# Kernel tuning notes

Hardware: AMD Instinct MI355X
Metric: run time of the kernel (lower is better)

## Reference

```python
import jax, jax.numpy as jnp
import numpy as np

L, B, S, D, H, F = 4, 2, 2048, 768, 12, 3072
HD = D // H
EPS = 1e-5


def _ln(x, g, b):
    m = jnp.mean(x, axis=-1, keepdims=True)
    v = jnp.mean((x - m) ** 2, axis=-1, keepdims=True)
    return (x - m) * jax.lax.rsqrt(v + EPS) * g + b


def setup_inputs() -> dict:
    key = jax.random.key(0)
    ks = jax.random.split(key, 12)
    s = 0.02
    n = lambda k, shp: jax.random.normal(k, shp, jnp.float32) * s
    return {
        "inputs": jax.random.normal(ks[0], (B, S, D), jnp.float32),
        "attn_mask": jax.random.randint(ks[1], (B, S, S), 0, 2) == 1,
        "Wq": n(ks[2], (L, D, D)), "bq": jnp.zeros((L, D), jnp.float32),
        "Wk": n(ks[3], (L, D, D)), "bk": jnp.zeros((L, D), jnp.float32),
        "Wv": n(ks[4], (L, D, D)), "bv": jnp.zeros((L, D), jnp.float32),
        "Wo": n(ks[5], (L, D, D)), "bo": jnp.zeros((L, D), jnp.float32),
        "ln1_g": jnp.ones((L, D), jnp.float32), "ln1_b": jnp.zeros((L, D), jnp.float32),
        "W1": n(ks[6], (L, F, D)), "b1": jnp.zeros((L, F), jnp.float32),
        "W2": n(ks[7], (L, D, F)), "b2": jnp.zeros((L, D), jnp.float32),
        "ln2_g": jnp.ones((L, D), jnp.float32), "ln2_b": jnp.zeros((L, D), jnp.float32),
    }


def reference(inputs, attn_mask, Wq, bq, Wk, bk, Wv, bv, Wo, bo,
              ln1_g, ln1_b, W1, b1, W2, b2, ln2_g, ln2_b):
    x = inputs
    scale = 1.0 / (HD ** 0.5)
    mask = attn_mask[:, None, :, :]  # [B,1,S,S] broadcasts over heads
    nlayers = Wq.shape[0]
    for i in range(nlayers):
        # torch Linear: y = x @ W.T + b, W stored [out,in]
        q = (jnp.einsum('bsd,ed->bse', x, Wq[i]) + bq[i]).reshape(B, S, H, HD)
        k = (jnp.einsum('bsd,ed->bse', x, Wk[i]) + bk[i]).reshape(B, S, H, HD)
        v = (jnp.einsum('bsd,ed->bse', x, Wv[i]) + bv[i]).reshape(B, S, H, HD)
        scores = jnp.einsum('bqhd,bkhd->bhqk', q, k) * scale
        scores = jnp.where(mask, jnp.float32(-1e9), scores)
        p = jax.nn.softmax(scores, axis=-1)
        ctx = jnp.einsum('bhqk,bkhd->bqhd', p, v).reshape(B, S, D)
        attn = jnp.einsum('bsd,ed->bse', ctx, Wo[i]) + bo[i]
        x = _ln(attn + x, ln1_g[i], ln1_b[i])
        h = jax.nn.relu(jnp.einsum('bsd,fd->bsf', x, W1[i]) + b1[i])
        ff = jnp.einsum('bsf,df->bsd', h, W2[i]) + b2[i]
        x = _ln(ff + x, ln2_g[i], ln2_b[i])
    return x
```

## Files before the change

### kernel.cpp

```cpp
#include <hip/hip_runtime.h>
#include <cmath>
#include <cstdint>
#include <cstddef>


typedef __bf16 bf16_t;
typedef __bf16 bf16x8 __attribute__((ext_vector_type(8)));
typedef __bf16 bf16x4 __attribute__((ext_vector_type(4)));
typedef float  f32x4  __attribute__((ext_vector_type(4)));
typedef float  f32x16 __attribute__((ext_vector_type(16)));
typedef int    i32x2  __attribute__((ext_vector_type(2)));

#define DEV static __device__ __forceinline__

constexpr int Lc = 4, Bc = 2, Sc = 2048, Dc = 768, Hc = 12, Fc = 3072, HDc = 64;
constexpr int Mrows = Bc * Sc;
#define QSCALE 0.18033688011112042f

DEV f32x4 mfma16(bf16x8 a, bf16x8 b, f32x4 c) {
  return __builtin_amdgcn_mfma_f32_16x16x32_bf16(a, b, c, 0, 0, 0);
}
DEV f32x16 mfma32(bf16x8 a, bf16x8 b, f32x16 c) {
  return __builtin_amdgcn_mfma_f32_32x32x16_bf16(a, b, c, 0, 0, 0);
}

DEV void gload_lds16(const void* g, void* l) {
  __builtin_amdgcn_global_load_lds(
      (const __attribute__((address_space(1))) void*)g,
      (__attribute__((address_space(3))) void*)l,
      16, 0, 0);
}

DEV float fexp2(float x) { return __builtin_amdgcn_exp2f(x); }

DEV unsigned cvtpk(float lo, float hi_) {
  unsigned r;
  asm("v_cvt_pk_bf16_f32 %0, %1, %2" : "=v"(r) : "v"(lo), "v"(hi_));
  return r;
}
DEV void swapl(unsigned &a, unsigned &b) {
  i32x2 r = __builtin_amdgcn_permlane32_swap((int)a, (int)b, false, false);
  a = (unsigned)r[0];
  b = (unsigned)r[1];
}
DEV bf16x8 frag4(unsigned a, unsigned b, unsigned c, unsigned d) {
  union { unsigned u[4]; bf16x8 v; } x;
  x.u[0] = a; x.u[1] = b; x.u[2] = c; x.u[3] = d;
  return x.v;
}


__global__ __launch_bounds__(256) void cvt_weights_kernel(
    const float* __restrict__ Wq, const float* __restrict__ Wk,
    const float* __restrict__ Wv, const float* __restrict__ Wo,
    const float* __restrict__ W1, const float* __restrict__ W2,
    bf16_t* __restrict__ wqkv, bf16_t* __restrict__ wo,
    bf16_t* __restrict__ w1, bf16_t* __restrict__ w2) {
  constexpr int DD = Dc * Dc;
  constexpr int nDD = Lc * DD;
  constexpr int nFD = Lc * Fc * Dc;
  int i = (blockIdx.x * 256 + threadIdx.x) * 4;
  const float* src;
  bf16_t* dst;
  if (i < 3 * nDD) {
    int sub = i / nDD, r = i - sub * nDD;
    int l = r / DD, off = r - l * DD;
    src = (sub == 0 ? Wq : (sub == 1 ? Wk : Wv)) + r;
    dst = wqkv + (size_t)(l * 3 + sub) * DD + off;
  } else if (i < 4 * nDD) {
    int r = i - 3 * nDD;
    src = Wo + r; dst = wo + r;
  } else if (i < 4 * nDD + nFD) {
    int r = i - 4 * nDD;
    src = W1 + r; dst = w1 + r;
  } else {
    int r = i - 4 * nDD - nFD;
    src = W2 + r; dst = w2 + r;
  }
  float4 v = *(const float4*)src;
  bf16x4 o;
  o[0] = (bf16_t)v.x; o[1] = (bf16_t)v.y; o[2] = (bf16_t)v.z; o[3] = (bf16_t)v.w;
  *(bf16x4*)dst = o;
}

__global__ __launch_bounds__(256) void init_x_kernel(const float* __restrict__ in,
                                                     float* __restrict__ x,
                                                     bf16_t* __restrict__ xb, int n) {
  int i = (blockIdx.x * 256 + threadIdx.x) * 4;
  if (i + 3 < n) {
    float4 v = *(const float4*)(in + i);
    *(float4*)(x + i) = v;
    bf16x4 o;
    o[0] = (bf16_t)v.x; o[1] = (bf16_t)v.y; o[2] = (bf16_t)v.z; o[3] = (bf16_t)v.w;
    *(bf16x4*)(xb + i) = o;
  }
}

__global__ __launch_bounds__(256) void mask_packT_kernel(const int* __restrict__ m,
                                                         unsigned long long* __restrict__ bits) {
  size_t gid = (size_t)blockIdx.x * 256 + threadIdx.x;
  int l = (int)(gid & 63);
  size_t widx = gid >> 6;
  size_t q = widx & (Sc - 1);
  size_t bkw = widx >> 11;
  size_t kw = bkw & (Sc / 64 - 1);
  size_t b = bkw >> 5;
  unsigned long long bm = __ballot(m[(b * Sc + q) * Sc + kw * 64 + l] != 0);
  if (l == 0) bits[widx] = bm;
}

__global__ __launch_bounds__(256) void gemm_ffn1(const bf16_t* __restrict__ A,
                                                 const bf16_t* __restrict__ Bm,
                                                 const float* __restrict__ bias,
                                                 bf16_t* __restrict__ Cb,
                                                 int M, int N, int K) {
  constexpr int BM = 128;
  __shared__ bf16_t sA[BM * 64];
  __shared__ bf16_t sB[128 * 64];
  const int tid = threadIdx.x;
  const int w = tid >> 6, l = tid & 63, lg = l >> 4, li = l & 15;
  const int wr = w >> 1, wc = w & 1;
  const int nwg = gridDim.x, cpx = nwg >> 3;
  const int id = blockIdx.x;
  const int tid2 = (id & 7) * cpx + (id >> 3);
  const int nbx = M / BM;
  const int tm = (tid2 % nbx) * BM, tn = (tid2 / nbx) * 128;

  f32x4 acc[4][4];
#pragma unroll
  for (int m = 0; m < 4; m++)
#pragma unroll
    for (int n = 0; n < 4; n++) acc[m][n] = (f32x4){0.f, 0.f, 0.f, 0.f};

  for (int k0 = 0; k0 < K; k0 += 64) {
#pragma unroll
    for (int i = 0; i < 4; i++) {
      int off = i * 2048 + tid * 8;
      gload_lds16(A + (size_t)(tm + (off >> 6)) * K + k0 + (off & 63),
                  &sA[i * 2048 + w * 512]);
    }
#pragma unroll
    for (int i = 0; i < 4; i++) {
      int off = i * 2048 + tid * 8;
      gload_lds16(Bm + (size_t)(tn + (off >> 6)) * K + k0 + (off & 63),
                  &sB[i * 2048 + w * 512]);
    }
    __syncthreads();
#pragma unroll
    for (int kk = 0; kk < 2; kk++) {
      bf16x8 af[4], bfr[4];
#pragma unroll
      for (int m = 0; m < 4; m++)
        af[m] = *(const bf16x8*)&sA[(wr * 64 + m * 16 + li) * 64 + kk * 32 + lg * 8];
#pragma unroll
      for (int n = 0; n < 4; n++)
        bfr[n] = *(const bf16x8*)&sB[(wc * 64 + n * 16 + li) * 64 + kk * 32 + lg * 8];
#pragma unroll
      for (int m = 0; m < 4; m++)
#pragma unroll
        for (int n = 0; n < 4; n++)
          acc[m][n] = mfma16(af[m], bfr[n], acc[m][n]);
    }
    __syncthreads();
  }

#pragma unroll
  for (int m = 0; m < 4; m++) {
    int rbase = tm + wr * 64 + m * 16 + lg * 4;
#pragma unroll
    for (int n = 0; n < 4; n++) {
      int c = tn + wc * 64 + n * 16 + li;
      float bv = bias[c];
#pragma unroll
      for (int j = 0; j < 4; j++)
        Cb[(size_t)(rbase + j) * N + c] = (bf16_t)fmaxf(acc[m][n][j] + bv, 0.f);
    }
  }
}

__global__ __launch_bounds__(256) void gemm_sk(const bf16_t* __restrict__ A,
                                               const bf16_t* __restrict__ Bm,
                                               float* __restrict__ P0,
                                               float* __restrict__ P1,
                                               int M, int N, int K) {
  __shared__ bf16_t sA[2 * 64 * 64];
  __shared__ bf16_t sB[2 * 128 * 64];
  const int tid = threadIdx.x;
  const int w = tid >> 6, l = tid & 63, lg = l >> 4, li = l & 15;
  const int wr = w >> 1, wc = w & 1;
  const int nwg = gridDim.x, cpx = nwg >> 3;
  const int id = blockIdx.x;
  const int tid2 = (id & 7) * cpx + (id >> 3);
  const int half = nwg >> 1;
  const int ks = tid2 >= half ? 1 : 0;
  const int r = tid2 - ks * half;
  const int nbx = M / 64;
  const int tm = (r % nbx) * 64, tn = (r / nbx) * 128;
  const int kB = K >> 1;
  const int k0base = ks * kB;
  const int nk = kB >> 6;
  float* __restrict__ P = ks ? P1 : P0;

  f32x4 acc[2][4];
#pragma unroll
  for (int m = 0; m < 2; m++)
#pragma unroll
    for (int n = 0; n < 4; n++) acc[m][n] = (f32x4){0.f, 0.f, 0.f, 0.f};

  auto stage = [&](int buf, int kt) {
    const int k0 = k0base + kt * 64;
#pragma unroll
    for (int i = 0; i < 2; i++) {
      int off = i * 2048 + tid * 8;
      gload_lds16(A + (size_t)(tm + (off >> 6)) * K + k0 + (off & 63),
                  &sA[buf * 4096 + i * 2048 + w * 512]);
    }
#pragma unroll
    for (int i = 0; i < 4; i++) {
      int off = i * 2048 + tid * 8;
      gload_lds16(Bm + (size_t)(tn + (off >> 6)) * K + k0 + (off & 63),
                  &sB[buf * 8192 + i * 2048 + w * 512]);
    }
  };

  stage(0, 0);
  asm volatile("s_waitcnt vmcnt(0)" ::: "memory");
  __builtin_amdgcn_s_barrier();
  asm volatile("" ::: "memory");
  int cur = 0;
  for (int kt = 0; kt < nk; kt++) {
    if (kt + 1 < nk) stage(cur ^ 1, kt + 1);
    const bf16_t* sAb = &sA[cur * 4096];
    const bf16_t* sBb = &sB[cur * 8192];
#pragma unroll
    for (int kk = 0; kk < 2; kk++) {
      bf16x8 af[2], bfr[4];
#pragma unroll
      for (int m = 0; m < 2; m++)
        af[m] = *(const bf16x8*)&sAb[(wr * 32 + m * 16 + li) * 64 + kk * 32 + lg * 8];
#pragma unroll
      for (int n = 0; n < 4; n++)
        bfr[n] = *(const bf16x8*)&sBb[(wc * 64 + n * 16 + li) * 64 + kk * 32 + lg * 8];
#pragma unroll
      for (int m = 0; m < 2; m++)
#pragma unroll
        for (int n = 0; n < 4; n++)
          acc[m][n] = mfma16(af[m], bfr[n], acc[m][n]);
    }
    asm volatile("s_waitcnt vmcnt(0)" ::: "memory");
    __builtin_amdgcn_s_barrier();
    asm volatile("" ::: "memory");
    cur ^= 1;
  }

#pragma unroll
  for (int m = 0; m < 2; m++) {
    int rbase = tm + wr * 32 + m * 16 + lg * 4;
#pragma unroll
    for (int n = 0; n < 4; n++) {
      int c = tn + wc * 64 + n * 16 + li;
#pragma unroll
      for (int j = 0; j < 4; j++)
        P[(size_t)(rbase + j) * N + c] = acc[m][n][j];
    }
  }
}

__global__ __launch_bounds__(256) void gemm_qkv(const bf16_t* __restrict__ A,
                                                const bf16_t* __restrict__ Bm,
                                                const float* __restrict__ bq,
                                                const float* __restrict__ bk,
                                                const float* __restrict__ bv,
                                                bf16_t* __restrict__ qo,
                                                bf16_t* __restrict__ ko,
                                                bf16_t* __restrict__ vTo) {
  constexpr int K = Dc;
  __shared__ bf16_t sA[128 * 64];
  __shared__ bf16_t sB[128 * 64];
  const int tid = threadIdx.x;
  const int w = tid >> 6, l = tid & 63, lg = l >> 4, li = l & 15;
  const int wr = w >> 1, wc = w & 1;
  const int nwg = gridDim.x, cpx = nwg >> 3;
  const int id = blockIdx.x;
  const int tid2 = (id & 7) * cpx + (id >> 3);
  constexpr int nbx = Mrows / 128;
  const int tm = (tid2 % nbx) * 128, tn = (tid2 / nbx) * 128;

  f32x4 acc[4][4];
#pragma unroll
  for (int m = 0; m < 4; m++)
#pragma unroll
    for (int n = 0; n < 4; n++) acc[m][n] = (f32x4){0.f, 0.f, 0.f, 0.f};

  for (int k0 = 0; k0 < K; k0 += 64) {
#pragma unroll
    for (int i = 0; i < 4; i++) {
      int off = i * 2048 + tid * 8;
      gload_lds16(A + (size_t)(tm + (off >> 6)) * K + k0 + (off & 63),
                  &sA[i * 2048 + w * 512]);
    }
#pragma unroll
    for (int i = 0; i < 4; i++) {
      int off = i * 2048 + tid * 8;
      gload_lds16(Bm + (size_t)(tn + (off >> 6)) * K + k0 + (off & 63),
                  &sB[i * 2048 + w * 512]);
    }
    __syncthreads();
#pragma unroll
    for (int kk = 0; kk < 2; kk++) {
      bf16x8 af[4], bfr[4];
#pragma unroll
      for (int m = 0; m < 4; m++)
        af[m] = *(const bf16x8*)&sA[(wr * 64 + m * 16 + li) * 64 + kk * 32 + lg * 8];
#pragma unroll
      for (int n = 0; n < 4; n++)
        bfr[n] = *(const bf16x8*)&sB[(wc * 64 + n * 16 + li) * 64 + kk * 32 + lg * 8];
#pragma unroll
      for (int m = 0; m < 4; m++)
#pragma unroll
        for (int n = 0; n < 4; n++)
          acc[m][n] = mfma16(af[m], bfr[n], acc[m][n]);
    }
    __syncthreads();
  }

  const int which = tn / 768;
#pragma unroll
  for (int m = 0; m < 4; m++) {
    int rbase = tm + wr * 64 + m * 16 + lg * 4;
#pragma unroll
    for (int n = 0; n < 4; n++) {
      int c = tn + wc * 64 + n * 16 + li;
      int col = c - which * 768;
      if (which == 0) {
        float bvv = bq[col];
#pragma unroll
        for (int j = 0; j < 4; j++)
          qo[(size_t)(rbase + j) * Dc + col] = (bf16_t)((acc[m][n][j] + bvv) * QSCALE);
      } else if (which == 1) {
        float bvv = bk[col];
#pragma unroll
        for (int j = 0; j < 4; j++)
          ko[(size_t)(rbase + j) * Dc + col] = (bf16_t)(acc[m][n][j] + bvv);
      } else {
        float bvv = bv[col];
        int h = col >> 6, d = col & 63;
        int b = rbase >> 11, s0 = rbase & 2047;
        bf16x4 pk;
#pragma unroll
        for (int j = 0; j < 4; j++) pk[j] = (bf16_t)(acc[m][n][j] + bvv);
        *(bf16x4*)(vTo + ((size_t)(b * Hc + h) * HDc + d) * Sc + s0) = pk;
      }
    }
  }
}

__global__ __launch_bounds__(256) void attn7_kernel(
    const bf16_t* __restrict__ q, const bf16_t* __restrict__ k,
    const bf16_t* __restrict__ vT, const unsigned long long* __restrict__ maskT,
    bf16_t* __restrict__ ctx) {
  __shared__ __align__(16) char smem[32768];

  const int t = threadIdx.x, w = t >> 6, l = t & 63;
  const int hi = l >> 5, li = l & 31;
  const int wp = w & 1, kvh = w >> 1;
  const int gid = blockIdx.x;
  const int tid2 = (gid & 7) * 96 + (gid >> 3);
  const int bh = tid2 >> 5, qt = tid2 & 31;
  const int b = bh / Hc, h = bh - b * Hc;
  const int qrow = qt * 64 + wp * 32 + li;

  const bf16_t* qp = q + (size_t)(b * Sc + qrow) * Dc + h * HDc + hi * 8;
  bf16x8 qf[4];
#pragma unroll
  for (int dk = 0; dk < 4; dk++) qf[dk] = *(const bf16x8*)(qp + dk * 16);

  const bf16_t* kg = k + ((size_t)(b * Sc) + kvh * 1024) * Dc + h * HDc;
  const bf16_t* vg = vT + (size_t)bh * HDc * Sc + kvh * 1024;
  const unsigned long long* mg =
      maskT + (size_t)b * 32 * Sc + (size_t)(kvh * 16) * Sc + qrow;

  f32x16 o0, o1;
#pragma unroll
  for (int r = 0; r < 16; r++) { o0[r] = 0.f; o1[r] = 0.f; }
  float ps = 0.f;

  auto stage = [&](int buf, int c) {
    const int kv0 = c * 32;
    bf16_t* sk = (bf16_t*)(smem + kvh * 16384 + buf * 8192);
    bf16_t* sv = (bf16_t*)(smem + kvh * 16384 + buf * 8192 + 4096);
#pragma unroll
    for (int i = 0; i < 2; i++) {
      int s = i * 128 + wp * 64 + l;
      int row = s >> 3, ch = s & 7;
      gload_lds16(kg + (size_t)(kv0 + row) * Dc + ((ch ^ (row & 7)) * 8),
                  sk + (i * 128 + wp * 64) * 8);
    }
#pragma unroll
    for (int i = 0; i < 2; i++) {
      int s = i * 128 + wp * 64 + l;
      int row = s >> 2, ch = s & 3;
      gload_lds16(vg + (size_t)row * Sc + kv0 + ((ch ^ ((row >> 1) & 3)) * 8),
                  sv + (i * 128 + wp * 64) * 8);
    }
  };

  stage(0, 0);
  __syncthreads();
  int cur = 0;
  unsigned long long mw = 0;
#pragma unroll 2
  for (int c = 0; c < 32; c++) {
    if (c + 1 < 32) stage(cur ^ 1, c + 1);
    if ((c & 1) == 0) mw = mg[(size_t)(c >> 1) * Sc];
    unsigned msel = (c & 1) ? (unsigned)(mw >> 32) : (unsigned)mw;
    unsigned ms0 = msel >> (hi * 4);

    f32x16 sc0;
#pragma unroll
    for (int r = 0; r < 16; r++) sc0[r] = 0.f;
    const bf16_t* kb = (const bf16_t*)(smem + kvh * 16384 + cur * 8192);
    __builtin_amdgcn_s_setprio(1);
#pragma unroll
    for (int dk = 0; dk < 4; dk++) {
      int ch = dk * 2 + hi;
      bf16x8 ka0 = *(const bf16x8*)(kb + li * 64 + ((ch ^ (li & 7)) * 8));
      sc0 = mfma32(ka0, qf[dk], sc0);
    }
    __builtin_amdgcn_s_setprio(0);

    unsigned pw[8];
#pragma unroll
    for (int r = 0; r < 16; r += 2) {
      int kbit = (r & 3) + 8 * (r >> 2);
      float a0 = fexp2(sc0[r]), a1 = fexp2(sc0[r + 1]);
      a0 = ((ms0 >> kbit) & 1u) ? 0.f : a0;
      a1 = ((ms0 >> (kbit + 1)) & 1u) ? 0.f : a1;
      ps += a0 + a1;
      pw[r >> 1] = cvtpk(a0, a1);
    }
    swapl(pw[0], pw[2]);  swapl(pw[1], pw[3]);
    swapl(pw[4], pw[6]);  swapl(pw[5], pw[7]);
    bf16x8 pb0 = frag4(pw[0], pw[1], pw[2], pw[3]);
    bf16x8 pb1 = frag4(pw[4], pw[5], pw[6], pw[7]);

    const bf16_t* vb = (const bf16_t*)(smem + kvh * 16384 + cur * 8192 + 4096);
    __builtin_amdgcn_s_setprio(1);
#pragma unroll
    for (int g = 0; g < 2; g++) {
      int ch = g * 2 + hi;
      bf16x8 va0 = *(const bf16x8*)(vb + li * 32 + ((ch ^ ((li >> 1) & 3)) * 8));
      bf16x8 va1 = *(const bf16x8*)(vb + (32 + li) * 32 + ((ch ^ ((li >> 1) & 3)) * 8));
      bf16x8 pbg = (g == 0) ? pb0 : pb1;
      o0 = mfma32(va0, pbg, o0);
      o1 = mfma32(va1, pbg, o1);
    }
    __builtin_amdgcn_s_setprio(0);
    __syncthreads();
    cur ^= 1;
  }

  float* mp = (float*)(smem + 16384);
  if (kvh == 1) {
    char* base = smem + wp * 8192 + l * 128;
#pragma unroll
    for (int r = 0; r < 4; r++) {
      *(f32x4*)(base + ((r ^ (l & 7)) * 16)) =
          (f32x4){o0[r * 4], o0[r * 4 + 1], o0[r * 4 + 2], o0[r * 4 + 3]};
      *(f32x4*)(base + (((r + 4) ^ (l & 7)) * 16)) =
          (f32x4){o1[r * 4], o1[r * 4 + 1], o1[r * 4 + 2], o1[r * 4 + 3]};
    }
    mp[wp * 64 + l] = ps;
  }
  __syncthreads();
  float inv = 0.f;
  if (kvh == 0) {
    char* base = smem + wp * 8192 + l * 128;
#pragma unroll
    for (int r = 0; r < 4; r++) {
      f32x4 u = *(const f32x4*)(base + ((r ^ (l & 7)) * 16));
      f32x4 v = *(const f32x4*)(base + (((r + 4) ^ (l & 7)) * 16));
#pragma unroll
      for (int j = 0; j < 4; j++) { o0[r * 4 + j] += u[j]; o1[r * 4 + j] += v[j]; }
    }
    ps += mp[wp * 64 + l];
    float tot = ps + __shfl_xor(ps, 32, 64);
    inv = 1.f / tot;
  }
  __syncthreads();
  if (kvh == 0) {
    char* so = smem + wp * 4096;
    const int lx = li & 7;
#pragma unroll
    for (int g = 0; g < 4; g++) {
      unsigned u0 = cvtpk(o0[g * 4 + 0] * inv, o0[g * 4 + 1] * inv);
      unsigned u1 = cvtpk(o0[g * 4 + 2] * inv, o0[g * 4 + 3] * inv);
      unsigned v0 = cvtpk(o1[g * 4 + 0] * inv, o1[g * 4 + 1] * inv);
      unsigned v1 = cvtpk(o1[g * 4 + 2] * inv, o1[g * 4 + 3] * inv);
      *(uint2*)(so + li * 128 + ((g ^ lx) * 16) + hi * 8) = make_uint2(u0, u1);
      *(uint2*)(so + li * 128 + (((g + 4) ^ lx) * 16) + hi * 8) = make_uint2(v0, v1);
    }
    __builtin_amdgcn_s_waitcnt(0);
    bf16_t* cbase = ctx + (size_t)(b * Sc + qt * 64 + wp * 32) * Dc + h * HDc;
#pragma unroll
    for (int i = 0; i < 4; i++) {
      int s = i * 64 + l;
      int row = s >> 3, ch = s & 7;
      bf16x8 vv = *(const bf16x8*)(so + row * 128 + ((ch ^ (row & 7)) * 16));
      *(bf16x8*)(cbase + (size_t)row * Dc + ch * 8) = vv;
    }
  }
}

__global__ __launch_bounds__(256) void ln_fuse_kernel(const float* __restrict__ p0,
                                                      const float* __restrict__ p1,
                                                      const float* __restrict__ bias,
                                                      const float* res,
                                                      const float* __restrict__ g,
                                                      const float* __restrict__ bb,
                                                      float* xo, bf16_t* __restrict__ xb) {
  const int row = blockIdx.x;
  const int t = threadIdx.x;
  const size_t base = (size_t)row * Dc;
  float v0 = p0[base + t] + p1[base + t] + bias[t] + res[base + t];
  float v1 = p0[base + t + 256] + p1[base + t + 256] + bias[t + 256] + res[base + t + 256];
  float v2 = p0[base + t + 512] + p1[base + t + 512] + bias[t + 512] + res[base + t + 512];
  float s = v0 + v1 + v2;
  float sq = v0 * v0 + v1 * v1 + v2 * v2;
#pragma unroll
  for (int ofs = 1; ofs < 64; ofs <<= 1) {
    s += __shfl_xor(s, ofs, 64);
    sq += __shfl_xor(sq, ofs, 64);
  }
  __shared__ float red[8];
  const int w = t >> 6, l = t & 63;
  if (l == 0) { red[w] = s; red[4 + w] = sq; }
  __syncthreads();
  s = red[0] + red[1] + red[2] + red[3];
  sq = red[4] + red[5] + red[6] + red[7];
  const float mean = s * (1.f / Dc);
  const float var = sq * (1.f / Dc) - mean * mean;
  const float rs = rsqrtf(var + 1e-5f);
  float* po = xo + base;
  bf16_t* pb = xb + base;
#pragma unroll
  for (int i = 0; i < 3; i++) {
    int d = t + i * 256;
    float vv = (i == 0 ? v0 : (i == 1 ? v1 : v2));
    float ov = (vv - mean) * rs * g[d] + bb[d];
    po[d] = ov;
    pb[d] = (bf16_t)ov;
  }
}


extern "C" void kernel_launch(void* const* d_in, const int* in_sizes, int n_in,
                              void* d_out, int out_size, void* d_ws, size_t ws_size,
                              hipStream_t stream) {
  const float* inputs = (const float*)d_in[0];
  const int* amask = (const int*)d_in[1];
  const float* Wq = (const float*)d_in[2];
  const float* bq = (const float*)d_in[3];
  const float* Wk = (const float*)d_in[4];
  const float* bk = (const float*)d_in[5];
  const float* Wv = (const float*)d_in[6];
  const float* bv = (const float*)d_in[7];
  const float* Wo = (const float*)d_in[8];
  const float* bo = (const float*)d_in[9];
  const float* ln1_g = (const float*)d_in[10];
  const float* ln1_b = (const float*)d_in[11];
  const float* W1 = (const float*)d_in[12];
  const float* b1 = (const float*)d_in[13];
  const float* W2 = (const float*)d_in[14];
  const float* b2 = (const float*)d_in[15];
  const float* ln2_g = (const float*)d_in[16];
  const float* ln2_b = (const float*)d_in[17];
  float* xout = (float*)d_out;

  char* p = (char*)d_ws;
  auto carve = [&](size_t bytes) -> char* {
    char* r = p;
    p += (bytes + 255) & ~(size_t)255;
    return r;
  };
  const size_t nDD = (size_t)Lc * Dc * Dc;
  const size_t nFD = (size_t)Lc * Fc * Dc;
  const size_t nAct = (size_t)Mrows * Dc;
  const size_t nHid = (size_t)Mrows * Fc;

  bf16_t* wqkv16 = (bf16_t*)carve(nDD * 3 * 2);
  bf16_t* wo16 = (bf16_t*)carve(nDD * 2);
  bf16_t* w1_16 = (bf16_t*)carve(nFD * 2);
  bf16_t* w2_16 = (bf16_t*)carve(nFD * 2);
  bf16_t* xb = (bf16_t*)carve(nAct * 2);
  bf16_t* q16 = (bf16_t*)carve(nAct * 2);
  bf16_t* k16 = (bf16_t*)carve(nAct * 2);
  bf16_t* vTb = (bf16_t*)carve(nAct * 2);
  bf16_t* ctx = (bf16_t*)carve(nAct * 2);
  bf16_t* h16 = (bf16_t*)carve(nHid * 2);
  float* attnf = (float*)carve(nAct * 4);
  float* ff = (float*)carve(nAct * 4);
  unsigned long long* maskb = (unsigned long long*)carve((size_t)Bc * (Sc / 64) * Sc * 8);
  (void)ws_size; (void)n_in; (void)in_sizes; (void)out_size;

  dim3 blk(256);

  mask_packT_kernel<<<(int)((size_t)Bc * Sc * Sc / 256), blk, 0, stream>>>(amask, maskb);
  cvt_weights_kernel<<<(int)((4 * nDD + 2 * nFD) / 1024), blk, 0, stream>>>(
      Wq, Wk, Wv, Wo, W1, W2, wqkv16, wo16, w1_16, w2_16);
  init_x_kernel<<<(int)(nAct / 1024), blk, 0, stream>>>(inputs, xout, xb, (int)nAct);

  for (int i = 0; i < Lc; i++) {
    const bf16_t* wqkv_l = wqkv16 + (size_t)i * 3 * Dc * Dc;
    const bf16_t* wo_l = wo16 + (size_t)i * Dc * Dc;
    const bf16_t* w1_l = w1_16 + (size_t)i * Fc * Dc;
    const bf16_t* w2_l = w2_16 + (size_t)i * Dc * Fc;

    gemm_qkv<<<576, blk, 0, stream>>>(
        xb, wqkv_l, bq + (size_t)i * Dc, bk + (size_t)i * Dc, bv + (size_t)i * Dc,
        q16, k16, vTb);

    attn7_kernel<<<768, blk, 0, stream>>>(q16, k16, vTb, maskb, ctx);

    gemm_sk<<<768, blk, 0, stream>>>(ctx, wo_l, attnf, ff, Mrows, Dc, Dc);
    ln_fuse_kernel<<<Mrows, blk, 0, stream>>>(attnf, ff, bo + (size_t)i * Dc, xout,
                                              ln1_g + (size_t)i * Dc,
                                              ln1_b + (size_t)i * Dc, xout, xb);
    gemm_ffn1<<<768, blk, 0, stream>>>(
        xb, w1_l, b1 + (size_t)i * Fc, h16, Mrows, Fc, Dc);
    gemm_sk<<<768, blk, 0, stream>>>(h16, w2_l, attnf, ff, Mrows, Dc, Fc);
    ln_fuse_kernel<<<Mrows, blk, 0, stream>>>(attnf, ff, b2 + (size_t)i * Dc, xout,
                                              ln2_g + (size_t)i * Dc,
                                              ln2_b + (size_t)i * Dc, xout, xb);
  }
}
```

Before: 865.5 us.

## Double-buffer LDS and halve M tile in QKV and FFN1 GEMMs

```diff
diff --git a/kernel.cpp b/kernel.cpp
--- a/kernel.cpp
+++ b/kernel.cpp
@@ -114,59 +114,73 @@
                                                  const float* __restrict__ bias,
                                                  bf16_t* __restrict__ Cb,
                                                  int M, int N, int K) {
-  constexpr int BM = 128;
-  __shared__ bf16_t sA[BM * 64];
-  __shared__ bf16_t sB[128 * 64];
+  __shared__ bf16_t sA[2 * 64 * 64];
+  __shared__ bf16_t sB[2 * 128 * 64];
   const int tid = threadIdx.x;
   const int w = tid >> 6, l = tid & 63, lg = l >> 4, li = l & 15;
   const int wr = w >> 1, wc = w & 1;
   const int nwg = gridDim.x, cpx = nwg >> 3;
   const int id = blockIdx.x;
   const int tid2 = (id & 7) * cpx + (id >> 3);
-  const int nbx = M / BM;
-  const int tm = (tid2 % nbx) * BM, tn = (tid2 / nbx) * 128;
-
-  f32x4 acc[4][4];
-#pragma unroll
-  for (int m = 0; m < 4; m++)
+  const int nbx = M / 64;
+  const int tm = (tid2 % nbx) * 64, tn = (tid2 / nbx) * 128;
+  const int nk = K >> 6;
+
+  f32x4 acc[2][4];
+#pragma unroll
+  for (int m = 0; m < 2; m++)
 #pragma unroll
     for (int n = 0; n < 4; n++) acc[m][n] = (f32x4){0.f, 0.f, 0.f, 0.f};
 
-  for (int k0 = 0; k0 < K; k0 += 64) {
-#pragma unroll
-    for (int i = 0; i < 4; i++) {
+  auto stage = [&](int buf, int kt) {
+    const int k0 = kt * 64;
+#pragma unroll
+    for (int i = 0; i < 2; i++) {
       int off = i * 2048 + tid * 8;
       gload_lds16(A + (size_t)(tm + (off >> 6)) * K + k0 + (off & 63),
-                  &sA[i * 2048 + w * 512]);
+                  &sA[buf * 4096 + i * 2048 + w * 512]);
     }
 #pragma unroll
     for (int i = 0; i < 4; i++) {
       int off = i * 2048 + tid * 8;
       gload_lds16(Bm + (size_t)(tn + (off >> 6)) * K + k0 + (off & 63),
-                  &sB[i * 2048 + w * 512]);
-    }
-    __syncthreads();
+                  &sB[buf * 8192 + i * 2048 + w * 512]);
+    }
+  };
+
+  stage(0, 0);
+  asm volatile("s_waitcnt vmcnt(0)" ::: "memory");
+  __builtin_amdgcn_s_barrier();
+  asm volatile("" ::: "memory");
+  int cur = 0;
+  for (int kt = 0; kt < nk; kt++) {
+    if (kt + 1 < nk) stage(cur ^ 1, kt + 1);
+    const bf16_t* sAb = &sA[cur * 4096];
+    const bf16_t* sBb = &sB[cur * 8192];
 #pragma unroll
     for (int kk = 0; kk < 2; kk++) {
-      bf16x8 af[4], bfr[4];
-#pragma unroll
-      for (int m = 0; m < 4; m++)
-        af[m] = *(const bf16x8*)&sA[(wr * 64 + m * 16 + li) * 64 + kk * 32 + lg * 8];
+      bf16x8 af[2], bfr[4];
+#pragma unroll
+      for (int m = 0; m < 2; m++)
+        af[m] = *(const bf16x8*)&sAb[(wr * 32 + m * 16 + li) * 64 + kk * 32 + lg * 8];
 #pragma unroll
       for (int n = 0; n < 4; n++)
-        bfr[n] = *(const bf16x8*)&sB[(wc * 64 + n * 16 + li) * 64 + kk * 32 + lg * 8];
-#pragma unroll
-      for (int m = 0; m < 4; m++)
+        bfr[n] = *(const bf16x8*)&sBb[(wc * 64 + n * 16 + li) * 64 + kk * 32 + lg * 8];
+#pragma unroll
+      for (int m = 0; m < 2; m++)
 #pragma unroll
         for (int n = 0; n < 4; n++)
           acc[m][n] = mfma16(af[m], bfr[n], acc[m][n]);
     }
-    __syncthreads();
-  }
-
-#pragma unroll
-  for (int m = 0; m < 4; m++) {
-    int rbase = tm + wr * 64 + m * 16 + lg * 4;
+    asm volatile("s_waitcnt vmcnt(0)" ::: "memory");
+    __builtin_amdgcn_s_barrier();
+    asm volatile("" ::: "memory");
+    cur ^= 1;
+  }
+
+#pragma unroll
+  for (int m = 0; m < 2; m++) {
+    int rbase = tm + wr * 32 + m * 16 + lg * 4;
 #pragma unroll
     for (int n = 0; n < 4; n++) {
       int c = tn + wc * 64 + n * 16 + li;
@@ -275,59 +289,74 @@
                                                 bf16_t* __restrict__ ko,
                                                 bf16_t* __restrict__ vTo) {
   constexpr int K = Dc;
-  __shared__ bf16_t sA[128 * 64];
-  __shared__ bf16_t sB[128 * 64];
+  __shared__ bf16_t sA[2 * 64 * 64];
+  __shared__ bf16_t sB[2 * 128 * 64];
   const int tid = threadIdx.x;
   const int w = tid >> 6, l = tid & 63, lg = l >> 4, li = l & 15;
   const int wr = w >> 1, wc = w & 1;
   const int nwg = gridDim.x, cpx = nwg >> 3;
   const int id = blockIdx.x;
   const int tid2 = (id & 7) * cpx + (id >> 3);
-  constexpr int nbx = Mrows / 128;
-  const int tm = (tid2 % nbx) * 128, tn = (tid2 / nbx) * 128;
-
-  f32x4 acc[4][4];
-#pragma unroll
-  for (int m = 0; m < 4; m++)
+  constexpr int nbx = Mrows / 64;
+  const int tm = (tid2 % nbx) * 64, tn = (tid2 / nbx) * 128;
+  constexpr int nk = K >> 6;
+
+  f32x4 acc[2][4];
+#pragma unroll
+  for (int m = 0; m < 2; m++)
 #pragma unroll
     for (int n = 0; n < 4; n++) acc[m][n] = (f32x4){0.f, 0.f, 0.f, 0.f};
 
-  for (int k0 = 0; k0 < K; k0 += 64) {
-#pragma unroll
-    for (int i = 0; i < 4; i++) {
+  auto stage = [&](int buf, int kt) {
+    const int k0 = kt * 64;
+#pragma unroll
+    for (int i = 0; i < 2; i++) {
       int off = i * 2048 + tid * 8;
       gload_lds16(A + (size_t)(tm + (off >> 6)) * K + k0 + (off & 63),
-                  &sA[i * 2048 + w * 512]);
+                  &sA[buf * 4096 + i * 2048 + w * 512]);
     }
 #pragma unroll
     for (int i = 0; i < 4; i++) {
       int off = i * 2048 + tid * 8;
       gload_lds16(Bm + (size_t)(tn + (off >> 6)) * K + k0 + (off & 63),
-                  &sB[i * 2048 + w * 512]);
-    }
-    __syncthreads();
+                  &sB[buf * 8192 + i * 2048 + w * 512]);
+    }
+  };
+
+  stage(0, 0);
+  asm volatile("s_waitcnt vmcnt(0)" ::: "memory");
+  __builtin_amdgcn_s_barrier();
+  asm volatile("" ::: "memory");
+  int cur = 0;
+  for (int kt = 0; kt < nk; kt++) {
+    if (kt + 1 < nk) stage(cur ^ 1, kt + 1);
+    const bf16_t* sAb = &sA[cur * 4096];
+    const bf16_t* sBb = &sB[cur * 8192];
 #pragma unroll
     for (int kk = 0; kk < 2; kk++) {
-      bf16x8 af[4], bfr[4];
-#pragma unroll
-      for (int m = 0; m < 4; m++)
-        af[m] = *(const bf16x8*)&sA[(wr * 64 + m * 16 + li) * 64 + kk * 32 + lg * 8];
+      bf16x8 af[2], bfr[4];
+#pragma unroll
+      for (int m = 0; m < 2; m++)
+        af[m] = *(const bf16x8*)&sAb[(wr * 32 + m * 16 + li) * 64 + kk * 32 + lg * 8];
 #pragma unroll
       for (int n = 0; n < 4; n++)
-        bfr[n] = *(const bf16x8*)&sB[(wc * 64 + n * 16 + li) * 64 + kk * 32 + lg * 8];
-#pragma unroll
-      for (int m = 0; m < 4; m++)
+        bfr[n] = *(const bf16x8*)&sBb[(wc * 64 + n * 16 + li) * 64 + kk * 32 + lg * 8];
+#pragma unroll
+      for (int m = 0; m < 2; m++)
 #pragma unroll
         for (int n = 0; n < 4; n++)
           acc[m][n] = mfma16(af[m], bfr[n], acc[m][n]);
     }
-    __syncthreads();
+    asm volatile("s_waitcnt vmcnt(0)" ::: "memory");
+    __builtin_amdgcn_s_barrier();
+    asm volatile("" ::: "memory");
+    cur ^= 1;
   }
 
   const int which = tn / 768;
 #pragma unroll
-  for (int m = 0; m < 4; m++) {
-    int rbase = tm + wr * 64 + m * 16 + lg * 4;
+  for (int m = 0; m < 2; m++) {
+    int rbase = tm + wr * 32 + m * 16 + lg * 4;
 #pragma unroll
     for (int n = 0; n < 4; n++) {
       int c = tn + wc * 64 + n * 16 + li;
@@ -616,7 +645,7 @@
     const bf16_t* w1_l = w1_16 + (size_t)i * Fc * Dc;
     const bf16_t* w2_l = w2_16 + (size_t)i * Dc * Fc;
 
-    gemm_qkv<<<576, blk, 0, stream>>>(
+    gemm_qkv<<<1152, blk, 0, stream>>>(
         xb, wqkv_l, bq + (size_t)i * Dc, bk + (size_t)i * Dc, bv + (size_t)i * Dc,
         q16, k16, vTb);
 
@@ -626,7 +655,7 @@
     ln_fuse_kernel<<<Mrows, blk, 0, stream>>>(attnf, ff, bo + (size_t)i * Dc, xout,
                                               ln1_g + (size_t)i * Dc,
                                               ln1_b + (size_t)i * Dc, xout, xb);
-    gemm_ffn1<<<768, blk, 0, stream>>>(
+    gemm_ffn1<<<1536, blk, 0, stream>>>(
         xb, w1_l, b1 + (size_t)i * Fc, h16, Mrows, Fc, Dc);
     gemm_sk<<<768, blk, 0, stream>>>(h16, w2_l, attnf, ff, Mrows, Dc, Fc);
     ln_fuse_kernel<<<Mrows, blk, 0, stream>>>(attnf, ff, b2 + (size_t)i * Dc, xout,
```

Result: faster. 800.7 us (-7.5%).
